# Optimization experiments

Hardware: AMD Instinct MI355X
Metric: run time of the kernel (lower is better)

The kernel has to match this reference:

```python
import jax, jax.numpy as jnp
import numpy as np

CODEBOOK_SIZE = 1024
D_MODEL = 512
NUM_SAMPLES = 10
TEMP = 1.0
COMMITMENT_COST = 0.25
PADDING_IDX = 0


def setup_inputs() -> dict:
    key = jax.random.key(0)
    k1, k2, k3 = jax.random.split(key, 3)
    inputs = jax.random.normal(k1, (64, 512, D_MODEL), dtype=jnp.float32)
    padding_mask = jax.random.randint(k2, (64, 512), 0, 2) == 1
    codebook_weight = 0.02 * jax.random.normal(k3, (CODEBOOK_SIZE, D_MODEL), dtype=jnp.float32)
    codebook_weight = codebook_weight.at[PADDING_IDX].set(0.0)  # padding_idx row zeroed
    return {"inputs": inputs, "padding_mask": padding_mask, "codebook_weight": codebook_weight}


def reference(inputs, padding_mask, codebook_weight):
    B, S, D = inputs.shape
    K = codebook_weight.shape[0]
    flat = inputs.reshape(-1, D)  # [N, D]
    # squared-euclidean distances to codebook entries: [N, K]
    dist = (jnp.sum(flat * flat, axis=1, keepdims=True)
            + jnp.sum(codebook_weight * codebook_weight, axis=1)
            - 2.0 * (flat @ codebook_weight.T))
    pad = padding_mask.reshape(-1)  # [N]
    col = jnp.arange(K)
    # padded rows: only code 0 allowed; non-padded rows: code 0 disallowed
    allowed = jnp.where(pad[:, None], col == 0, col != 0)
    dist = jnp.where(allowed, dist, jnp.inf)

    # Multinomial(total_count=NUM_SAMPLES, logits=-dist/TEMP): draw NUM_SAMPLES
    # categorical samples per row and count them.
    logits = -dist / TEMP
    N = flat.shape[0]
    draws = jax.random.categorical(jax.random.key(42), logits, axis=-1,
                                   shape=(NUM_SAMPLES, N))  # [num_samples, N]
    row_idx = jnp.broadcast_to(jnp.arange(N)[None, :], draws.shape)
    samples = jnp.zeros((N, K), jnp.float32).at[row_idx, draws].add(1.0)  # counts, [N, K]

    quantized = (samples @ codebook_weight).reshape(B, S, D) / NUM_SAMPLES

    num_nonpad = (jnp.sum(~pad) * D).astype(jnp.float32)
    e_latent_loss = jnp.sum((jax.lax.stop_gradient(quantized) - inputs) ** 2) / num_nonpad
    loss = COMMITMENT_COST * e_latent_loss

    # straight-through estimator
    quantized_st = inputs + jax.lax.stop_gradient(quantized - inputs)

    avg_probs = jnp.mean(samples, axis=0) / NUM_SAMPLES  # [K]
    perplexity = jnp.exp(-jnp.sum(avg_probs * jnp.log(avg_probs + 1e-10)))

    samples_out = samples.reshape(B, S, K)
    return quantized_st, samples_out, loss, perplexity
```

## Files before the change

### kernel.cpp

```cpp
#include <hip/hip_runtime.h>
#include <stdint.h>

#define NROWS 32768
#define KC 1024
#define DM 512
#define NKPROD 33554432u

typedef _Float16 v8h __attribute__((ext_vector_type(8)));
typedef float v4f __attribute__((ext_vector_type(4)));

__device__ __forceinline__ uint32_t rotl32(uint32_t x, int d) {
  return __builtin_amdgcn_alignbit(x, x, 32 - d);
}

__device__ __forceinline__ void threefry(uint32_t x0, uint32_t x1,
                                         uint32_t& o0, uint32_t& o1) {
  const uint32_t ks0 = 0u, ks1 = 42u, ks2 = 0x1BD11BF0u;
  x0 += ks0; x1 += ks1;
#define TFR(r) { x0 += x1; x1 = rotl32(x1, r); x1 ^= x0; }
  TFR(13) TFR(15) TFR(26) TFR(6)
  x0 += ks1; x1 += ks2 + 1u;
  TFR(17) TFR(29) TFR(16) TFR(24)
  x0 += ks2; x1 += ks0 + 2u;
  TFR(13) TFR(15) TFR(26) TFR(6)
  x0 += ks0; x1 += ks1 + 3u;
  TFR(17) TFR(29) TFR(16) TFR(24)
  x0 += ks1; x1 += ks2 + 4u;
  TFR(13) TFR(15) TFR(26) TFR(6)
  x0 += ks2; x1 += ks0 + 5u;
#undef TFR
  o0 = x0; o1 = x1;
}

__global__ __launch_bounds__(1024) void k_prep(const void* __restrict__ mv,
                                               uint8_t* __restrict__ wm,
                                               int* __restrict__ idx,
                                               int* __restrict__ npp) {
  __shared__ uint32_t sflag;
  __shared__ int scnt[1024];
  int t = threadIdx.x;
  if (t == 0) sflag = 0;
  __syncthreads();
  const uint8_t* mb = (const uint8_t*)mv;
  uint32_t f = 0;
  for (int i = t; i < NROWS; i += 1024)
    if ((i & 3) && mb[i]) f = 1;
  if (f) atomicOr(&sflag, 1u);
  __syncthreads();
  bool isbool = sflag != 0;

  int r0 = t * 32;
  int cnt = 0;
  for (int i = 0; i < 32; ++i) {
    int r = r0 + i;
    bool p = isbool ? (mb[r] != 0) : (((const int*)mv)[r] != 0);
    wm[r] = p ? 1u : 0u;
    cnt += p ? 0 : 1;
  }
  scnt[t] = cnt;
  __syncthreads();
  for (int off = 1; off < 1024; off <<= 1) {
    int v = (t >= off) ? scnt[t - off] : 0;
    __syncthreads();
    scnt[t] += v;
    __syncthreads();
  }
  int pos = scnt[t] - cnt;
  for (int i = 0; i < 32; ++i) {
    int r = r0 + i;
    bool p = isbool ? (mb[r] != 0) : (((const int*)mv)[r] != 0);
    if (!p) idx[pos++] = r;
  }
  if (t == 1023) *npp = scnt[1023];
}

__global__ __launch_bounds__(256) void k_pad(const float* __restrict__ X,
                                             const uint8_t* __restrict__ wm,
                                             float* __restrict__ qout,
                                             float* __restrict__ sout,
                                             double* __restrict__ esum) {
  int n = blockIdx.x * 4 + (threadIdx.x >> 6);
  int l = threadIdx.x & 63;
  if (!wm[n]) return;

  float* so = sout + (size_t)n * KC + l * 16;
  float4 z = make_float4(0.f, 0.f, 0.f, 0.f);
  *(float4*)(so)      = (l == 0) ? make_float4(10.f, 0.f, 0.f, 0.f) : z;
  *(float4*)(so + 4)  = z;
  *(float4*)(so + 8)  = z;
  *(float4*)(so + 12) = z;

  const float* xr = X + (size_t)n * DM + l * 8;
  float4 x0 = *(const float4*)xr, x1 = *(const float4*)(xr + 4);
  float* qo = qout + (size_t)n * DM + l * 8;
  *(float4*)qo       = z;
  *(float4*)(qo + 4) = z;
  double ls = (double)(x0.x*x0.x) + (double)(x0.y*x0.y)
            + (double)(x0.z*x0.z) + (double)(x0.w*x0.w)
            + (double)(x1.x*x1.x) + (double)(x1.y*x1.y)
            + (double)(x1.z*x1.z) + (double)(x1.w*x1.w);
#pragma unroll
  for (int off = 32; off; off >>= 1) ls += __shfl_xor(ls, off, 64);
  if (l == 0) atomicAdd(&esum[n & 63], ls);
}

__global__ __launch_bounds__(64) void k_cnorm(const float* __restrict__ B,
                                              float* __restrict__ cn) {
  int k = blockIdx.x, l = threadIdx.x;
  const float* bp = B + (size_t)k * DM + l * 8;
  float4 v0 = *(const float4*)bp, v1 = *(const float4*)(bp + 4);
  float s = v0.x*v0.x + v0.y*v0.y + v0.z*v0.z + v0.w*v0.w
          + v1.x*v1.x + v1.y*v1.y + v1.z*v1.z + v1.w*v1.w;
#pragma unroll
  for (int off = 32; off; off >>= 1) s += __shfl_xor(s, off, 64);
  if (l == 0) cn[k] = s;
}

#define LDK 40
__global__ __launch_bounds__(256) void k_gemm2i(const float* __restrict__ A,
                                                const float* __restrict__ B,
                                                const float* __restrict__ cn,
                                                const int* __restrict__ idx,
                                                const int* __restrict__ npp,
                                                float* __restrict__ S) {
  int NP = *npp;
  int bx = blockIdx.x & 7;
  int by = blockIdx.x >> 3;
  int r0 = by * 128, c0 = bx * 128;
  if (r0 >= NP) return;

  __shared__ _Float16 Ah[128 * LDK], Al[128 * LDK];
  __shared__ _Float16 Bh[128 * LDK], Bl[128 * LDK];
  __shared__ float rs[128];
  __shared__ float tmp[256];

  int tid = threadIdx.x;
  int wid = tid >> 6;
  int wr = wid >> 1, wc = wid & 1;
  int l = tid & 63;
  int lr = l & 15;
  int k8 = (l >> 4) * 8;

  int srow = tid >> 1;
  int ssub = (tid & 1) * 16;

  int slot = r0 + srow;
  int orig = idx[slot < NP ? slot : NP - 1];
  const float* ag = A + (size_t)orig * DM + ssub;
  const float* bg = B + (size_t)(c0 + srow) * DM + ssub;

  v4f acc[4][4];
#pragma unroll
  for (int m = 0; m < 4; ++m)
#pragma unroll
    for (int n = 0; n < 4; ++n) acc[m][n] = (v4f)0.0f;

  float sqa = 0.f;

  for (int k0 = 0; k0 < DM; k0 += 32) {
    float xa[16], xb[16];
#pragma unroll
    for (int i = 0; i < 16; i += 4) {
      *(float4*)&xa[i] = *(const float4*)(ag + k0 + i);
      *(float4*)&xb[i] = *(const float4*)(bg + k0 + i);
    }
    _Float16 ha[16], la[16], hb[16], lb[16];
#pragma unroll
    for (int i = 0; i < 16; ++i) {
      float x = xa[i];
      _Float16 h = (_Float16)x;
      ha[i] = h; la[i] = (_Float16)(x - (float)h);
      sqa = fmaf(x, x, sqa);
      float y = xb[i];
      _Float16 g = (_Float16)y;
      hb[i] = g; lb[i] = (_Float16)(y - (float)g);
    }
    __syncthreads();
    int wb = srow * LDK + ssub;
    *(v8h*)&Ah[wb]     = *(v8h*)&ha[0];
    *(v8h*)&Ah[wb + 8] = *(v8h*)&ha[8];
    *(v8h*)&Al[wb]     = *(v8h*)&la[0];
    *(v8h*)&Al[wb + 8] = *(v8h*)&la[8];
    *(v8h*)&Bh[wb]     = *(v8h*)&hb[0];
    *(v8h*)&Bh[wb + 8] = *(v8h*)&hb[8];
    *(v8h*)&Bl[wb]     = *(v8h*)&lb[0];
    *(v8h*)&Bl[wb + 8] = *(v8h*)&lb[8];
    __syncthreads();

    v8h fah[4], fal[4];
#pragma unroll
    for (int m = 0; m < 4; ++m) {
      int row = wr * 64 + m * 16 + lr;
      fah[m] = *(const v8h*)&Ah[row * LDK + k8];
      fal[m] = *(const v8h*)&Al[row * LDK + k8];
    }
#pragma unroll
    for (int n = 0; n < 4; ++n) {
      int col = wc * 64 + n * 16 + lr;
      v8h fbh = *(const v8h*)&Bh[col * LDK + k8];
      v8h fbl = *(const v8h*)&Bl[col * LDK + k8];
#pragma unroll
      for (int m = 0; m < 4; ++m) {
        acc[m][n] = __builtin_amdgcn_mfma_f32_16x16x32_f16(fah[m], fbh, acc[m][n], 0, 0, 0);
        acc[m][n] = __builtin_amdgcn_mfma_f32_16x16x32_f16(fah[m], fbl, acc[m][n], 0, 0, 0);
        acc[m][n] = __builtin_amdgcn_mfma_f32_16x16x32_f16(fal[m], fbh, acc[m][n], 0, 0, 0);
      }
    }
  }

  tmp[tid] = sqa;
  __syncthreads();
  if ((tid & 1) == 0) rs[srow] = tmp[tid] + tmp[tid + 1];
  __syncthreads();

  float cnp[4];
#pragma unroll
  for (int n = 0; n < 4; ++n) cnp[n] = cn[c0 + wc * 64 + n * 16 + lr];

#pragma unroll
  for (int m = 0; m < 4; ++m) {
    int rl = wr * 64 + m * 16 + (l >> 4) * 4;
#pragma unroll
    for (int r = 0; r < 4; ++r) {
      int sl = r0 + rl + r;
      int org = idx[sl < NP ? sl : NP - 1];
      float rq = rs[rl + r];
      float* sp = S + (size_t)org * KC + c0;
#pragma unroll
      for (int n = 0; n < 4; ++n) {
        int cl = wc * 64 + n * 16 + lr;
        sp[cl] = -((rq + cnp[n]) - 2.0f * acc[m][n][r]);
      }
    }
  }
}

__global__ __launch_bounds__(256, 4) void k_sample_i(
    const float* __restrict__ S, const float* __restrict__ X,
    const float* __restrict__ CW, const int* __restrict__ idx,
    const int* __restrict__ npp,
    float* __restrict__ qout, float* __restrict__ sout,
    float* __restrict__ cnt, double* __restrict__ esum) {
  int NP = *npp;
  int slot = blockIdx.x * 4 + (threadIdx.x >> 6);
  if (slot >= NP) return;
  int n = idx[slot];
  int l = threadIdx.x & 63;
  int base = l * 16;
  const float* srow = S + (size_t)n * KC + base;

  float lmax;
  {
    float lg0[16];
#pragma unroll
    for (int j = 0; j < 16; j += 4)
      *(float4*)&lg0[j] = *(const float4*)(srow + j);
    if (l == 0) lg0[0] = -__builtin_inff();
    lmax = lg0[0];
#pragma unroll
    for (int i = 1; i < 16; ++i) lmax = fmaxf(lmax, lg0[i]);
#pragma unroll
    for (int off = 32; off; off >>= 1)
      lmax = fmaxf(lmax, __shfl_xor(lmax, off, 64));
  }

  float bv[10];
  uint32_t bi[10];
#pragma unroll
  for (int s = 0; s < 10; ++s) { bv[s] = -__builtin_inff(); bi[s] = 0xFFFFFFFFu; }

  uint32_t tb0 = (uint32_t)n * (uint32_t)KC + (uint32_t)base;
#pragma unroll 1
  for (int j = 0; j < 16; ++j) {
    float lgj = srow[j];
    uint32_t kk = (uint32_t)(base + j);
    if (kk == 0u) lgj = -__builtin_inff();
    float mj = 0.69314718056f * __expf(lmax - lgj);
    uint32_t t0 = tb0 + (uint32_t)j;
#pragma unroll
    for (int s = 0; s < 10; ++s) {
      uint32_t o0, o1;
      threefry(0u, t0 + (uint32_t)s * NKPROD, o0, o1);
      uint32_t b = o0 ^ o1;
      float f = __uint_as_float((b >> 9) | 0x3F800000u) - 1.0f;
      float u = fmaxf(1.17549435e-38f, f);
      float v = __log2f(u) * mj;
      if (v > bv[s]) { bv[s] = v; bi[s] = kk; }
    }
  }

#pragma unroll
  for (int s = 0; s < 10; ++s) {
#pragma unroll
    for (int off = 32; off; off >>= 1) {
      float ov = __shfl_xor(bv[s], off, 64);
      uint32_t oi = __shfl_xor(bi[s], off, 64);
      if (ov > bv[s] || (ov == bv[s] && oi < bi[s])) { bv[s] = ov; bi[s] = oi; }
    }
  }

  float* so = sout + (size_t)n * KC + base;
#pragma unroll
  for (int j4 = 0; j4 < 16; j4 += 4) {
    float c[4];
#pragma unroll
    for (int i = 0; i < 4; ++i) {
      uint32_t k = (uint32_t)(base + j4 + i);
      float cc = 0.f;
#pragma unroll
      for (int s = 0; s < 10; ++s) cc += (bi[s] == k) ? 1.f : 0.f;
      c[i] = cc;
    }
    *(float4*)(so + j4) = make_float4(c[0], c[1], c[2], c[3]);
  }

  float q[8];
#pragma unroll
  for (int i = 0; i < 8; ++i) q[i] = 0.f;
#pragma unroll
  for (int s = 0; s < 10; ++s) {
    const float* cr = CW + (size_t)bi[s] * DM + l * 8;
    float4 g0 = *(const float4*)cr;
    float4 g1 = *(const float4*)(cr + 4);
    q[0] += g0.x; q[1] += g0.y; q[2] += g0.z; q[3] += g0.w;
    q[4] += g1.x; q[5] += g1.y; q[6] += g1.z; q[7] += g1.w;
    if (l == 0) atomicAdd(&cnt[bi[s]], 1.0f);
  }

  const float* xr = X + (size_t)n * DM + l * 8;
  float4 x0 = *(const float4*)xr, x1 = *(const float4*)(xr + 4);
  float xs[8] = {x0.x, x0.y, x0.z, x0.w, x1.x, x1.y, x1.z, x1.w};
  float st[8];
  double ls = 0.0;
#pragma unroll
  for (int j = 0; j < 8; ++j) {
    float qq = q[j] / 10.0f;
    float d = qq - xs[j];
    ls += (double)(d * d);
    st[j] = xs[j] + d;
  }
  float* qo = qout + (size_t)n * DM + l * 8;
  *(float4*)qo       = make_float4(st[0], st[1], st[2], st[3]);
  *(float4*)(qo + 4) = make_float4(st[4], st[5], st[6], st[7]);

#pragma unroll
  for (int off = 32; off; off >>= 1) ls += __shfl_xor(ls, off, 64);
  if (l == 0) atomicAdd(&esum[n & 63], ls);
}

__global__ __launch_bounds__(256) void k_final(const uint8_t* __restrict__ wm,
                                               const float* __restrict__ cnt,
                                               const double* __restrict__ esum,
                                               float* __restrict__ scal) {
  __shared__ int sni[256];
  __shared__ double snd[256];
  int t = threadIdx.x;
  int np = 0;
  for (int i = t; i < NROWS; i += 256) np += wm[i];
  sni[t] = np;
  __syncthreads();
  for (int off = 128; off; off >>= 1) {
    if (t < off) sni[t] += sni[t + off];
    __syncthreads();
  }
  int npad = sni[0];
  double ss = 0.0;
  for (int k = t; k < KC; k += 256) {
    float c = (k == 0) ? (float)(npad * 10) : cnt[k];
    float p = c / 327680.0f;
    ss += (double)(p * logf(p + 1e-10f));
  }
  snd[t] = ss;
  __syncthreads();
  for (int off = 128; off; off >>= 1) {
    if (t < off) snd[t] += snd[t + off];
    __syncthreads();
  }
  if (t == 0) {
    double es = 0.0;
    for (int i = 0; i < 64; ++i) es += esum[i];
    float num_nonpad = (float)((NROWS - npad) * DM);
    float el = (float)es / num_nonpad;
    scal[0] = 0.25f * el;
    scal[1] = expf(-(float)snd[0]);
  }
}

extern "C" void kernel_launch(void* const* d_in, const int* in_sizes, int n_in,
                              void* d_out, int out_size, void* d_ws, size_t ws_size,
                              hipStream_t stream) {
  const float* X  = (const float*)d_in[0];
  const void*  M  = d_in[1];
  const float* CW = (const float*)d_in[2];
  float* out  = (float*)d_out;
  float* qout = out;
  float* sout = out + 16777216;
  float* scal = out + 50331648;
  uint8_t* ws = (uint8_t*)d_ws;
  double*   esum = (double*)ws;
  float*    cnt  = (float*)(ws + 1024);
  uint8_t*  wm   = ws + 8192;
  float*    cng  = (float*)(ws + 40960);
  int*      npp  = (int*)(ws + 45056);
  int*      idx  = (int*)(ws + 49152);
  (void)in_sizes; (void)n_in; (void)out_size; (void)ws_size;

  hipMemsetAsync(d_ws, 0, 8192, stream);
  k_prep<<<1, 1024, 0, stream>>>(M, wm, idx, npp);
  k_pad<<<8192, 256, 0, stream>>>(X, wm, qout, sout, esum);
  k_cnorm<<<KC, 64, 0, stream>>>(CW, cng);
  k_gemm2i<<<2048, 256, 0, stream>>>(X, CW, cng, idx, npp, sout);
  k_sample_i<<<8192, 256, 0, stream>>>(sout, X, CW, idx, npp, qout, sout, cnt, esum);
  k_final<<<1, 256, 0, stream>>>(wm, cnt, esum, scal);
}
```

Before: 572.6 us.

## Parallelize mask prep, fuse codebook norms into GEMM, interleave threefry pairs

Replaces the single-block prep kernel (with its serial scan) with a detect kernel plus a 64-block compaction that uses atomic counters. Folds the codebook-norm computation into the GEMM so the separate kernel goes away. Interleaves two threefry streams for more ILP, drops the zero-key adds, and raises the sampler's occupancy hint. Atomic compaction makes row order nondeterministic, which is safe for output correctness but can change memory locality. The GEMM also recomputes the norms redundantly across blocks.

```diff
diff --git a/kernel.cpp b/kernel.cpp
--- a/kernel.cpp
+++ b/kernel.cpp
@@ -13,65 +13,53 @@
   return __builtin_amdgcn_alignbit(x, x, 32 - d);
 }
 
-__device__ __forceinline__ void threefry(uint32_t x0, uint32_t x1,
-                                         uint32_t& o0, uint32_t& o1) {
-  const uint32_t ks0 = 0u, ks1 = 42u, ks2 = 0x1BD11BF0u;
-  x0 += ks0; x1 += ks1;
-#define TFR(r) { x0 += x1; x1 = rotl32(x1, r); x1 ^= x0; }
-  TFR(13) TFR(15) TFR(26) TFR(6)
-  x0 += ks1; x1 += ks2 + 1u;
-  TFR(17) TFR(29) TFR(16) TFR(24)
-  x0 += ks2; x1 += ks0 + 2u;
-  TFR(13) TFR(15) TFR(26) TFR(6)
-  x0 += ks0; x1 += ks1 + 3u;
-  TFR(17) TFR(29) TFR(16) TFR(24)
-  x0 += ks1; x1 += ks2 + 4u;
-  TFR(13) TFR(15) TFR(26) TFR(6)
-  x0 += ks2; x1 += ks0 + 5u;
-#undef TFR
-  o0 = x0; o1 = x1;
-}
-
-__global__ __launch_bounds__(1024) void k_prep(const void* __restrict__ mv,
+__device__ __forceinline__ void threefry_x2(uint32_t xa, uint32_t xb,
+                                            uint32_t& oa, uint32_t& ob) {
+  const uint32_t ks1 = 42u, ks2 = 0x1BD11BF0u;
+  uint32_t a0 = 0u, a1 = xa + ks1;
+  uint32_t b0 = 0u, b1 = xb + ks1;
+#define R2(r) { a0 += a1; b0 += b1; a1 = rotl32(a1, r); b1 = rotl32(b1, r); a1 ^= a0; b1 ^= b0; }
+  R2(13) R2(15) R2(26) R2(6)
+  a0 += ks1; b0 += ks1; a1 += ks2 + 1u; b1 += ks2 + 1u;
+  R2(17) R2(29) R2(16) R2(24)
+  a0 += ks2; b0 += ks2; a1 += 2u; b1 += 2u;
+  R2(13) R2(15) R2(26) R2(6)
+  a1 += ks1 + 3u; b1 += ks1 + 3u;
+  R2(17) R2(29) R2(16) R2(24)
+  a0 += ks1; b0 += ks1; a1 += ks2 + 4u; b1 += ks2 + 4u;
+  R2(13) R2(15) R2(26) R2(6)
+  a0 += ks2; b0 += ks2; a1 += 5u; b1 += 5u;
+#undef R2
+  oa = a0 ^ a1;
+  ob = b0 ^ b1;
+}
+
+__global__ __launch_bounds__(256) void k_detect(const uint8_t* __restrict__ m,
+                                                uint32_t* __restrict__ flag) {
+  uint32_t f = 0;
+  for (int i = threadIdx.x; i < NROWS; i += 256)
+    if ((i & 3) && m[i]) f = 1;
+  if (f) atomicOr(flag, 1u);
+}
+
+__global__ __launch_bounds__(256) void k_prep2(const void* __restrict__ mv,
+                                               const uint32_t* __restrict__ flag,
                                                uint8_t* __restrict__ wm,
                                                int* __restrict__ idx,
                                                int* __restrict__ npp) {
-  __shared__ uint32_t sflag;
-  __shared__ int scnt[1024];
-  int t = threadIdx.x;
-  if (t == 0) sflag = 0;
-  __syncthreads();
+  bool isbool = (*flag) != 0;
+  int t = blockIdx.x * 256 + threadIdx.x;
   const uint8_t* mb = (const uint8_t*)mv;
-  uint32_t f = 0;
-  for (int i = t; i < NROWS; i += 1024)
-    if ((i & 3) && mb[i]) f = 1;
-  if (f) atomicOr(&sflag, 1u);
-  __syncthreads();
-  bool isbool = sflag != 0;
-
-  int r0 = t * 32;
-  int cnt = 0;
-  for (int i = 0; i < 32; ++i) {
-    int r = r0 + i;
+#pragma unroll
+  for (int i = 0; i < 2; ++i) {
+    int r = t * 2 + i;
     bool p = isbool ? (mb[r] != 0) : (((const int*)mv)[r] != 0);
     wm[r] = p ? 1u : 0u;
-    cnt += p ? 0 : 1;
-  }
-  scnt[t] = cnt;
-  __syncthreads();
-  for (int off = 1; off < 1024; off <<= 1) {
-    int v = (t >= off) ? scnt[t - off] : 0;
-    __syncthreads();
-    scnt[t] += v;
-    __syncthreads();
-  }
-  int pos = scnt[t] - cnt;
-  for (int i = 0; i < 32; ++i) {
-    int r = r0 + i;
-    bool p = isbool ? (mb[r] != 0) : (((const int*)mv)[r] != 0);
-    if (!p) idx[pos++] = r;
-  }
-  if (t == 1023) *npp = scnt[1023];
+    if (!p) {
+      int pos = atomicAdd(npp, 1);
+      idx[pos] = r;
+    }
+  }
 }
 
 __global__ __launch_bounds__(256) void k_pad(const float* __restrict__ X,
@@ -104,22 +92,9 @@
   if (l == 0) atomicAdd(&esum[n & 63], ls);
 }
 
-__global__ __launch_bounds__(64) void k_cnorm(const float* __restrict__ B,
-                                              float* __restrict__ cn) {
-  int k = blockIdx.x, l = threadIdx.x;
-  const float* bp = B + (size_t)k * DM + l * 8;
-  float4 v0 = *(const float4*)bp, v1 = *(const float4*)(bp + 4);
-  float s = v0.x*v0.x + v0.y*v0.y + v0.z*v0.z + v0.w*v0.w
-          + v1.x*v1.x + v1.y*v1.y + v1.z*v1.z + v1.w*v1.w;
-#pragma unroll
-  for (int off = 32; off; off >>= 1) s += __shfl_xor(s, off, 64);
-  if (l == 0) cn[k] = s;
-}
-
 #define LDK 40
 __global__ __launch_bounds__(256) void k_gemm2i(const float* __restrict__ A,
                                                 const float* __restrict__ B,
-                                                const float* __restrict__ cn,
                                                 const int* __restrict__ idx,
                                                 const int* __restrict__ npp,
                                                 float* __restrict__ S) {
@@ -132,6 +107,7 @@
   __shared__ _Float16 Ah[128 * LDK], Al[128 * LDK];
   __shared__ _Float16 Bh[128 * LDK], Bl[128 * LDK];
   __shared__ float rs[128];
+  __shared__ float cs[128];
   __shared__ float tmp[256];
 
   int tid = threadIdx.x;
@@ -155,7 +131,7 @@
 #pragma unroll
     for (int n = 0; n < 4; ++n) acc[m][n] = (v4f)0.0f;
 
-  float sqa = 0.f;
+  float sqa = 0.f, sqb = 0.f;
 
   for (int k0 = 0; k0 < DM; k0 += 32) {
     float xa[16], xb[16];
@@ -174,6 +150,7 @@
       float y = xb[i];
       _Float16 g = (_Float16)y;
       hb[i] = g; lb[i] = (_Float16)(y - (float)g);
+      sqb = fmaf(y, y, sqb);
     }
     __syncthreads();
     int wb = srow * LDK + ssub;
@@ -212,10 +189,14 @@
   __syncthreads();
   if ((tid & 1) == 0) rs[srow] = tmp[tid] + tmp[tid + 1];
   __syncthreads();
+  tmp[tid] = sqb;
+  __syncthreads();
+  if ((tid & 1) == 0) cs[srow] = tmp[tid] + tmp[tid + 1];
+  __syncthreads();
 
   float cnp[4];
 #pragma unroll
-  for (int n = 0; n < 4; ++n) cnp[n] = cn[c0 + wc * 64 + n * 16 + lr];
+  for (int n = 0; n < 4; ++n) cnp[n] = cs[wc * 64 + n * 16 + lr];
 
 #pragma unroll
   for (int m = 0; m < 4; ++m) {
@@ -235,7 +216,7 @@
   }
 }
 
-__global__ __launch_bounds__(256, 4) void k_sample_i(
+__global__ __launch_bounds__(256, 8) void k_sample_i(
     const float* __restrict__ S, const float* __restrict__ X,
     const float* __restrict__ CW, const int* __restrict__ idx,
     const int* __restrict__ npp,
@@ -278,14 +259,18 @@
     float mj = 0.69314718056f * __expf(lmax - lgj);
     uint32_t t0 = tb0 + (uint32_t)j;
 #pragma unroll
-    for (int s = 0; s < 10; ++s) {
-      uint32_t o0, o1;
-      threefry(0u, t0 + (uint32_t)s * NKPROD, o0, o1);
-      uint32_t b = o0 ^ o1;
-      float f = __uint_as_float((b >> 9) | 0x3F800000u) - 1.0f;
-      float u = fmaxf(1.17549435e-38f, f);
-      float v = __log2f(u) * mj;
-      if (v > bv[s]) { bv[s] = v; bi[s] = kk; }
+    for (int sp = 0; sp < 5; ++sp) {
+      uint32_t ba, bb;
+      threefry_x2(t0 + (uint32_t)(2 * sp) * NKPROD,
+                  t0 + (uint32_t)(2 * sp + 1) * NKPROD, ba, bb);
+      float fa = __uint_as_float((ba >> 9) | 0x3F800000u) - 1.0f;
+      float fb = __uint_as_float((bb >> 9) | 0x3F800000u) - 1.0f;
+      float ua = fmaxf(1.17549435e-38f, fa);
+      float ub = fmaxf(1.17549435e-38f, fb);
+      float va = __log2f(ua) * mj;
+      float vb = __log2f(ub) * mj;
+      if (va > bv[2 * sp])     { bv[2 * sp] = va;     bi[2 * sp] = kk; }
+      if (vb > bv[2 * sp + 1]) { bv[2 * sp + 1] = vb; bi[2 * sp + 1] = kk; }
     }
   }
 
@@ -398,18 +383,18 @@
   float* scal = out + 50331648;
   uint8_t* ws = (uint8_t*)d_ws;
   double*   esum = (double*)ws;
+  uint32_t* flag = (uint32_t*)(ws + 512);
+  int*      npp  = (int*)(ws + 768);
   float*    cnt  = (float*)(ws + 1024);
   uint8_t*  wm   = ws + 8192;
-  float*    cng  = (float*)(ws + 40960);
-  int*      npp  = (int*)(ws + 45056);
   int*      idx  = (int*)(ws + 49152);
   (void)in_sizes; (void)n_in; (void)out_size; (void)ws_size;
 
   hipMemsetAsync(d_ws, 0, 8192, stream);
-  k_prep<<<1, 1024, 0, stream>>>(M, wm, idx, npp);
+  k_detect<<<1, 256, 0, stream>>>((const uint8_t*)M, flag);
+  k_prep2<<<64, 256, 0, stream>>>(M, flag, wm, idx, npp);
   k_pad<<<8192, 256, 0, stream>>>(X, wm, qout, sout, esum);
-  k_cnorm<<<KC, 64, 0, stream>>>(CW, cng);
-  k_gemm2i<<<2048, 256, 0, stream>>>(X, CW, cng, idx, npp, sout);
+  k_gemm2i<<<2048, 256, 0, stream>>>(X, CW, idx, npp, sout);
   k_sample_i<<<8192, 256, 0, stream>>>(sout, X, CW, idx, npp, qout, sout, cnt, esum);
   k_final<<<1, 256, 0, stream>>>(wm, cnt, esum, scal);
 }
```

Result: no change. 567.5 us (-0.9%).

## Hand-schedule paired Threefry in asm, fold codebook norms into GEMM, raise occupancy

Applied to the files above, without the earlier changes.

Replaces the compiler-generated Threefry with an inline-asm version that interleaves two independent streams. It uses constant-folded key schedule values (x0 starts at 0, so the first round collapses) and equivalent right-rotate amounts, which should raise ILP and cut instructions in the RNG-bound sampling loop. Removes the separate codebook-norm kernel by accumulating squared codebook values inside the GEMM tile loads, which saves one launch at the cost of a few extra FMAs and barriers. Raises the sampling kernel's min-waves launch bound from 4 to 6, which may force register spills.

```diff
diff --git a/kernel.cpp b/kernel.cpp
--- a/kernel.cpp
+++ b/kernel.cpp
@@ -9,27 +9,54 @@
 typedef _Float16 v8h __attribute__((ext_vector_type(8)));
 typedef float v4f __attribute__((ext_vector_type(4)));
 
-__device__ __forceinline__ uint32_t rotl32(uint32_t x, int d) {
-  return __builtin_amdgcn_alignbit(x, x, 32 - d);
-}
-
-__device__ __forceinline__ void threefry(uint32_t x0, uint32_t x1,
-                                         uint32_t& o0, uint32_t& o1) {
-  const uint32_t ks0 = 0u, ks1 = 42u, ks2 = 0x1BD11BF0u;
-  x0 += ks0; x1 += ks1;
-#define TFR(r) { x0 += x1; x1 = rotl32(x1, r); x1 ^= x0; }
-  TFR(13) TFR(15) TFR(26) TFR(6)
-  x0 += ks1; x1 += ks2 + 1u;
-  TFR(17) TFR(29) TFR(16) TFR(24)
-  x0 += ks2; x1 += ks0 + 2u;
-  TFR(13) TFR(15) TFR(26) TFR(6)
-  x0 += ks0; x1 += ks1 + 3u;
-  TFR(17) TFR(29) TFR(16) TFR(24)
-  x0 += ks1; x1 += ks2 + 4u;
-  TFR(13) TFR(15) TFR(26) TFR(6)
-  x0 += ks2; x1 += ks0 + 5u;
-#undef TFR
-  o0 = x0; o1 = x1;
+#define TFR2(s) \
+  "v_add_u32 %0, %0, %1\n\t" \
+  "v_add_u32 %2, %2, %3\n\t" \
+  "v_alignbit_b32 %1, %1, %1, " #s "\n\t" \
+  "v_alignbit_b32 %3, %3, %3, " #s "\n\t" \
+  "v_xor_b32 %1, %0, %1\n\t" \
+  "v_xor_b32 %3, %2, %3\n\t"
+
+__device__ __forceinline__ void threefry_x2(uint32_t ta, uint32_t tb,
+                                            uint32_t& oa, uint32_t& ob) {
+  uint32_t a0, a1, b0, b1;
+  asm(
+      "v_add_u32 %1, 42, %4\n\t"
+      "v_add_u32 %3, 42, %5\n\t"
+      "v_mov_b32 %0, %1\n\t"
+      "v_mov_b32 %2, %3\n\t"
+      "v_alignbit_b32 %1, %1, %1, 19\n\t"
+      "v_alignbit_b32 %3, %3, %3, 19\n\t"
+      "v_xor_b32 %1, %0, %1\n\t"
+      "v_xor_b32 %3, %2, %3\n\t"
+      TFR2(17) TFR2(6) TFR2(26)
+      "v_add_u32 %0, 42, %0\n\t"
+      "v_add_u32 %2, 42, %2\n\t"
+      "v_add_u32 %1, 0x1BD11BF1, %1\n\t"
+      "v_add_u32 %3, 0x1BD11BF1, %3\n\t"
+      TFR2(15) TFR2(3) TFR2(16) TFR2(8)
+      "v_add_u32 %0, 0x1BD11BF0, %0\n\t"
+      "v_add_u32 %2, 0x1BD11BF0, %2\n\t"
+      "v_add_u32 %1, 2, %1\n\t"
+      "v_add_u32 %3, 2, %3\n\t"
+      TFR2(19) TFR2(17) TFR2(6) TFR2(26)
+      "v_add_u32 %1, 45, %1\n\t"
+      "v_add_u32 %3, 45, %3\n\t"
+      TFR2(15) TFR2(3) TFR2(16) TFR2(8)
+      "v_add_u32 %0, 42, %0\n\t"
+      "v_add_u32 %2, 42, %2\n\t"
+      "v_add_u32 %1, 0x1BD11BF4, %1\n\t"
+      "v_add_u32 %3, 0x1BD11BF4, %3\n\t"
+      TFR2(19) TFR2(17) TFR2(6) TFR2(26)
+      "v_add_u32 %0, 0x1BD11BF0, %0\n\t"
+      "v_add_u32 %2, 0x1BD11BF0, %2\n\t"
+      "v_add_u32 %1, 5, %1\n\t"
+      "v_add_u32 %3, 5, %3\n\t"
+      "v_xor_b32 %0, %0, %1\n\t"
+      "v_xor_b32 %2, %2, %3"
+      : "=&v"(a0), "=&v"(a1), "=&v"(b0), "=&v"(b1)
+      : "v"(ta), "v"(tb));
+  oa = a0; ob = b0;
 }
 
 __global__ __launch_bounds__(1024) void k_prep(const void* __restrict__ mv,
@@ -104,22 +131,9 @@
   if (l == 0) atomicAdd(&esum[n & 63], ls);
 }
 
-__global__ __launch_bounds__(64) void k_cnorm(const float* __restrict__ B,
-                                              float* __restrict__ cn) {
-  int k = blockIdx.x, l = threadIdx.x;
-  const float* bp = B + (size_t)k * DM + l * 8;
-  float4 v0 = *(const float4*)bp, v1 = *(const float4*)(bp + 4);
-  float s = v0.x*v0.x + v0.y*v0.y + v0.z*v0.z + v0.w*v0.w
-          + v1.x*v1.x + v1.y*v1.y + v1.z*v1.z + v1.w*v1.w;
-#pragma unroll
-  for (int off = 32; off; off >>= 1) s += __shfl_xor(s, off, 64);
-  if (l == 0) cn[k] = s;
-}
-
 #define LDK 40
 __global__ __launch_bounds__(256) void k_gemm2i(const float* __restrict__ A,
                                                 const float* __restrict__ B,
-                                                const float* __restrict__ cn,
                                                 const int* __restrict__ idx,
                                                 const int* __restrict__ npp,
                                                 float* __restrict__ S) {
@@ -132,6 +146,7 @@
   __shared__ _Float16 Ah[128 * LDK], Al[128 * LDK];
   __shared__ _Float16 Bh[128 * LDK], Bl[128 * LDK];
   __shared__ float rs[128];
+  __shared__ float cs[128];
   __shared__ float tmp[256];
 
   int tid = threadIdx.x;
@@ -155,7 +170,7 @@
 #pragma unroll
     for (int n = 0; n < 4; ++n) acc[m][n] = (v4f)0.0f;
 
-  float sqa = 0.f;
+  float sqa = 0.f, sqb = 0.f;
 
   for (int k0 = 0; k0 < DM; k0 += 32) {
     float xa[16], xb[16];
@@ -174,6 +189,7 @@
       float y = xb[i];
       _Float16 g = (_Float16)y;
       hb[i] = g; lb[i] = (_Float16)(y - (float)g);
+      sqb = fmaf(y, y, sqb);
     }
     __syncthreads();
     int wb = srow * LDK + ssub;
@@ -212,10 +228,14 @@
   __syncthreads();
   if ((tid & 1) == 0) rs[srow] = tmp[tid] + tmp[tid + 1];
   __syncthreads();
+  tmp[tid] = sqb;
+  __syncthreads();
+  if ((tid & 1) == 0) cs[srow] = tmp[tid] + tmp[tid + 1];
+  __syncthreads();
 
   float cnp[4];
 #pragma unroll
-  for (int n = 0; n < 4; ++n) cnp[n] = cn[c0 + wc * 64 + n * 16 + lr];
+  for (int n = 0; n < 4; ++n) cnp[n] = cs[wc * 64 + n * 16 + lr];
 
 #pragma unroll
   for (int m = 0; m < 4; ++m) {
@@ -235,7 +255,7 @@
   }
 }
 
-__global__ __launch_bounds__(256, 4) void k_sample_i(
+__global__ __launch_bounds__(256, 6) void k_sample_i(
     const float* __restrict__ S, const float* __restrict__ X,
     const float* __restrict__ CW, const int* __restrict__ idx,
     const int* __restrict__ npp,
@@ -278,14 +298,18 @@
     float mj = 0.69314718056f * __expf(lmax - lgj);
     uint32_t t0 = tb0 + (uint32_t)j;
 #pragma unroll
-    for (int s = 0; s < 10; ++s) {
-      uint32_t o0, o1;
-      threefry(0u, t0 + (uint32_t)s * NKPROD, o0, o1);
-      uint32_t b = o0 ^ o1;
-      float f = __uint_as_float((b >> 9) | 0x3F800000u) - 1.0f;
-      float u = fmaxf(1.17549435e-38f, f);
-      float v = __log2f(u) * mj;
-      if (v > bv[s]) { bv[s] = v; bi[s] = kk; }
+    for (int sp = 0; sp < 5; ++sp) {
+      uint32_t ba, bb;
+      threefry_x2(t0 + (uint32_t)(2 * sp) * NKPROD,
+                  t0 + (uint32_t)(2 * sp + 1) * NKPROD, ba, bb);
+      float fa = __uint_as_float((ba >> 9) | 0x3F800000u) - 1.0f;
+      float fb = __uint_as_float((bb >> 9) | 0x3F800000u) - 1.0f;
+      float ua = fmaxf(1.17549435e-38f, fa);
+      float ub = fmaxf(1.17549435e-38f, fb);
+      float va = __log2f(ua) * mj;
+      float vb = __log2f(ub) * mj;
+      if (va > bv[2 * sp])     { bv[2 * sp] = va;     bi[2 * sp] = kk; }
+      if (vb > bv[2 * sp + 1]) { bv[2 * sp + 1] = vb; bi[2 * sp + 1] = kk; }
     }
   }
 
@@ -400,7 +424,6 @@
   double*   esum = (double*)ws;
   float*    cnt  = (float*)(ws + 1024);
   uint8_t*  wm   = ws + 8192;
-  float*    cng  = (float*)(ws + 40960);
   int*      npp  = (int*)(ws + 45056);
   int*      idx  = (int*)(ws + 49152);
   (void)in_sizes; (void)n_in; (void)out_size; (void)ws_size;
@@ -408,8 +431,7 @@
   hipMemsetAsync(d_ws, 0, 8192, stream);
   k_prep<<<1, 1024, 0, stream>>>(M, wm, idx, npp);
   k_pad<<<8192, 256, 0, stream>>>(X, wm, qout, sout, esum);
-  k_cnorm<<<KC, 64, 0, stream>>>(CW, cng);
-  k_gemm2i<<<2048, 256, 0, stream>>>(X, CW, cng, idx, npp, sout);
+  k_gemm2i<<<2048, 256, 0, stream>>>(X, CW, idx, npp, sout);
   k_sample_i<<<8192, 256, 0, stream>>>(sout, X, CW, idx, npp, qout, sout, cnt, esum);
   k_final<<<1, 256, 0, stream>>>(wm, cnt, esum, scal);
 }
```

New measurement: 614.4 us. 1.07x slower.
